# Kernel tuning notes

Hardware: AMD Instinct MI355X
Metric: run time of the kernel (lower is better)

Reference implementation:

```python
import jax, jax.numpy as jnp
import numpy as np

F = 64      # input_v_size
E = 64      # emb_v_size
H = 8       # int(sqrt(emb_v_size))
P = 512     # proj_e_size
B, T = 64, 256


def setup_inputs() -> dict:
    key = jax.random.key(0)
    ks = jax.random.split(key, 14)
    s1 = 1.0            # Linear(1->H): fan_in=1
    s2 = 1.0 / np.sqrt(H)
    s3 = 1.0 / np.sqrt(F * E)
    return {
        "x":    jax.random.normal(ks[0], (B, T, F), dtype=jnp.float32),
        "time": jax.random.uniform(ks[1], (B, T, F), dtype=jnp.float32),
        # stacked per-feature Linear(1->H): weight [F,H], bias [F,H]
        "w1v": jax.random.uniform(ks[2], (F, H), jnp.float32, -s1, s1),
        "b1v": jax.random.uniform(ks[3], (F, H), jnp.float32, -s1, s1),
        # stacked per-feature Linear(H->E, bias=False): [F,H,E]
        "w2v": jax.random.uniform(ks[4], (F, H, E), jnp.float32, -s2, s2),
        "w1t": jax.random.uniform(ks[5], (F, H), jnp.float32, -s1, s1),
        "b1t": jax.random.uniform(ks[6], (F, H), jnp.float32, -s1, s1),
        "w2t": jax.random.uniform(ks[7], (F, H, E), jnp.float32, -s2, s2),
        # Wx, Wt: Linear(F*E -> P) stored as [F*E, P] (= torch weight.T)
        "wx":  jax.random.uniform(ks[8], (F * E, P), jnp.float32, -s3, s3),
        "bx":  jax.random.uniform(ks[9], (P,), jnp.float32, -s3, s3),
        "wt":  jax.random.uniform(ks[10], (F * E, P), jnp.float32, -s3, s3),
        "bt":  jax.random.uniform(ks[11], (P,), jnp.float32, -s3, s3),
    }


def _branch(inp, w1, b1, w2):
    # inp [B,T,F]; w1,b1 [F,H]; w2 [F,H,E]
    h = jnp.tanh(inp[..., None] * w1 + b1)          # [B,T,F,H]
    e = jnp.einsum("btfh,fhe->btfe", h, w2)          # [B,T,F,E]
    return e.reshape(*inp.shape[:2], -1)              # [B,T,F*E]


def reference(x, time, w1v, b1v, w2v, w1t, b1t, w2t, wx, bx, wt, bt):
    x_out = _branch(x, w1v, b1v, w2v)
    t_out = _branch(time, w1t, b1t, w2t)
    return (x_out @ wx + bx) + (t_out @ wt + bt)      # [B,T,P]
```

## Files before the change

kernel.cpp:

```cpp
#include <hip/hip_runtime.h>
#include <cstdint>
#include <cstddef>

#define FF 64
#define EE 64
#define HH 8
#define PP 512
#define MM 16384
#define KK 1024

typedef __bf16 bf16x8 __attribute__((ext_vector_type(8)));
typedef float  floatx4 __attribute__((ext_vector_type(4)));

__device__ __forceinline__ unsigned short f2bf(float f) {
    unsigned int u = __float_as_uint(f);
    u += 0x7FFFu + ((u >> 16) & 1u);
    return (unsigned short)(u >> 16);
}

__device__ __forceinline__ unsigned pack2(unsigned short a, unsigned short b) {
    return (unsigned)a | ((unsigned)b << 16);
}

__device__ __forceinline__ float fast_tanh_s(float t) {
    float e, r;
    asm("v_exp_f32 %0, %1" : "=v"(e) : "v"(t));
    float d = e + 1.0f;
    asm("v_rcp_f32 %0, %1" : "=v"(r) : "v"(d));
    return __builtin_fmaf(-2.0f, r, 1.0f);
}

__device__ __forceinline__ void gl_lds16(const unsigned short* g, unsigned short* s) {
    __builtin_amdgcn_global_load_lds(
        (__attribute__((address_space(1))) void*)(void*)g,
        (__attribute__((address_space(3))) void*)s,
        16, 0, 0);
}

__global__ __launch_bounds__(256) void combine_kernel(
    const float* __restrict__ w2v, const float* __restrict__ w2t,
    const float* __restrict__ wx,  const float* __restrict__ wt,
    unsigned short* __restrict__ BmatT)
{
    const int tid = threadIdx.x;
    const int bid = blockIdx.x;
    const int br = bid >> 7;
    const int f  = (bid >> 1) & 63;
    const int nh = bid & 1;
    const float* __restrict__ w2 = br ? w2t : w2v;
    const float* __restrict__ W  = br ? wt  : wx;
    __shared__ float w2s[HH * EE];
    for (int i = tid; i < HH * EE; i += 256) w2s[i] = w2[f * HH * EE + i];
    __syncthreads();
    const int n = nh * 256 + tid;
    float acc[HH] = {0,0,0,0,0,0,0,0};
    const float* Wcol = W + (size_t)f * EE * PP + n;
    #pragma unroll 8
    for (int e = 0; e < EE; ++e) {
        const float wv = Wcol[(size_t)e * PP];
        #pragma unroll
        for (int h = 0; h < HH; ++h)
            acc[h] = __builtin_fmaf(w2s[h * EE + e], wv, acc[h]);
    }
    uint4 v;
    v.x = pack2(f2bf(acc[0]), f2bf(acc[1]));
    v.y = pack2(f2bf(acc[2]), f2bf(acc[3]));
    v.z = pack2(f2bf(acc[4]), f2bf(acc[5]));
    v.w = pack2(f2bf(acc[6]), f2bf(acc[7]));
    *reinterpret_cast<uint4*>(&BmatT[(size_t)n * KK + br * 512 + f * 8]) = v;
}

__global__ __launch_bounds__(512, 4) void gemm_fused_kernel(
    const float* __restrict__ x,   const float* __restrict__ tmv,
    const float* __restrict__ w1v, const float* __restrict__ b1v,
    const float* __restrict__ w1t, const float* __restrict__ b1t,
    const unsigned short* __restrict__ Bt,
    const float* __restrict__ bx, const float* __restrict__ bt,
    float* __restrict__ out)
{
    __shared__ __align__(16) unsigned short As[64 * 64];
    __shared__ __align__(16) unsigned short Bs[256 * 64];
    __shared__ __align__(16) float w1s[2 * FF * HH];
    __shared__ __align__(16) float b1s[2 * FF * HH];

    const int tid  = threadIdx.x;
    const int wave = tid >> 6;
    const int lane = tid & 63;
    const int m0 = blockIdx.x * 64;
    const int n0 = blockIdx.y * 256;

    {
        const float c = 2.8853900817779268f;
        #pragma unroll
        for (int t = 0; t < 2; ++t) {
            const int idx = tid + t * 512;
            const int br  = idx >> 9;
            const int rem = idx & 511;
            w1s[idx] = (br ? w1t : w1v)[rem] * c;
            b1s[idx] = (br ? b1t : b1v)[rem] * c;
        }
    }
    __syncthreads();

    const int wm  = wave >> 2;
    const int wn  = wave & 3;
    const int q   = lane >> 4;
    const int ml  = lane & 15;
    const int mlx = ml & 7;
    const int lr  = lane >> 3;
    const int lkg = ((lane & 7) ^ lr) * 8;
    const int fi  = tid & 7;
    const int arow = tid >> 3;
    const int pchunk = (fi ^ (arow & 7)) * 8;

    floatx4 acc[2][4];
    #pragma unroll
    for (int i = 0; i < 2; ++i)
        #pragma unroll
        for (int j = 0; j < 4; ++j)
            acc[i][j] = (floatx4){0.f, 0.f, 0.f, 0.f};

    for (int k0 = 0; k0 < KK; k0 += 64) {
        const int br = k0 >> 9;
        const int f0 = (k0 >> 3) & 63;

        #pragma unroll
        for (int i = 0; i < 4; ++i) {
            const int seg = wave * 4 + i;
            gl_lds16(&Bt[(size_t)(n0 + seg * 8 + lr) * KK + k0 + lkg], &Bs[seg * 512]);
        }

        {
            const float* __restrict__ inp = br ? tmv : x;
            const int f = f0 + fi;
            const float val = inp[(size_t)(m0 + arow) * FF + f];
            const float4 wlo = reinterpret_cast<const float4*>(w1s)[br * 128 + f * 2];
            const float4 whi = reinterpret_cast<const float4*>(w1s)[br * 128 + f * 2 + 1];
            const float4 blo = reinterpret_cast<const float4*>(b1s)[br * 128 + f * 2];
            const float4 bhi = reinterpret_cast<const float4*>(b1s)[br * 128 + f * 2 + 1];
            float hv[8];
            hv[0] = fast_tanh_s(__builtin_fmaf(val, wlo.x, blo.x));
            hv[1] = fast_tanh_s(__builtin_fmaf(val, wlo.y, blo.y));
            hv[2] = fast_tanh_s(__builtin_fmaf(val, wlo.z, blo.z));
            hv[3] = fast_tanh_s(__builtin_fmaf(val, wlo.w, blo.w));
            hv[4] = fast_tanh_s(__builtin_fmaf(val, whi.x, bhi.x));
            hv[5] = fast_tanh_s(__builtin_fmaf(val, whi.y, bhi.y));
            hv[6] = fast_tanh_s(__builtin_fmaf(val, whi.z, bhi.z));
            hv[7] = fast_tanh_s(__builtin_fmaf(val, whi.w, bhi.w));
            uint4 v;
            v.x = pack2(f2bf(hv[0]), f2bf(hv[1]));
            v.y = pack2(f2bf(hv[2]), f2bf(hv[3]));
            v.z = pack2(f2bf(hv[4]), f2bf(hv[5]));
            v.w = pack2(f2bf(hv[6]), f2bf(hv[7]));
            *reinterpret_cast<uint4*>(&As[arow * 64 + pchunk]) = v;
        }
        __syncthreads();

        #pragma unroll
        for (int kk = 0; kk < 64; kk += 32) {
            const int cl = (kk >> 3) + q;
            const int co = (cl ^ mlx) * 8;
            bf16x8 af[2], bfr[4];
            #pragma unroll
            for (int mt = 0; mt < 2; ++mt)
                af[mt] = *reinterpret_cast<const bf16x8*>(
                    &As[(wm * 32 + mt * 16 + ml) * 64 + co]);
            #pragma unroll
            for (int nt = 0; nt < 4; ++nt)
                bfr[nt] = *reinterpret_cast<const bf16x8*>(
                    &Bs[(wn * 64 + nt * 16 + ml) * 64 + co]);
            #pragma unroll
            for (int mt = 0; mt < 2; ++mt)
                #pragma unroll
                for (int nt = 0; nt < 4; ++nt)
                    acc[mt][nt] = __builtin_amdgcn_mfma_f32_16x16x32_bf16(
                        af[mt], bfr[nt], acc[mt][nt], 0, 0, 0);
        }
        __syncthreads();
    }

    float bias[4];
    #pragma unroll
    for (int nt = 0; nt < 4; ++nt) {
        const int n = n0 + wn * 64 + nt * 16 + ml;
        bias[nt] = bx[n] + bt[n];
    }
    #pragma unroll
    for (int mt = 0; mt < 2; ++mt) {
        const int mb = m0 + wm * 32 + mt * 16 + q * 4;
        #pragma unroll
        for (int r = 0; r < 4; ++r) {
            float* orow = out + (size_t)(mb + r) * PP + n0 + wn * 64 + ml;
            #pragma unroll
            for (int nt = 0; nt < 4; ++nt)
                orow[nt * 16] = acc[mt][nt][r] + bias[nt];
        }
    }
}

extern "C" void kernel_launch(void* const* d_in, const int* in_sizes, int n_in,
                              void* d_out, int out_size, void* d_ws, size_t ws_size,
                              hipStream_t stream)
{
    const float* x   = (const float*)d_in[0];
    const float* tmv = (const float*)d_in[1];
    const float* w1v = (const float*)d_in[2];
    const float* b1v = (const float*)d_in[3];
    const float* w2v = (const float*)d_in[4];
    const float* w1t = (const float*)d_in[5];
    const float* b1t = (const float*)d_in[6];
    const float* w2t = (const float*)d_in[7];
    const float* wx  = (const float*)d_in[8];
    const float* bx  = (const float*)d_in[9];
    const float* wt  = (const float*)d_in[10];
    const float* bt  = (const float*)d_in[11];
    float* out = (float*)d_out;

    unsigned short* Bws = (unsigned short*)d_ws;

    combine_kernel<<<256, 256, 0, stream>>>(w2v, w2t, wx, wt, Bws);
    gemm_fused_kernel<<<dim3(MM / 64, PP / 256), 512, 0, stream>>>(
        x, tmv, w1v, b1v, w1t, b1t, Bws, bx, bt, out);
}
```

Measured before the change: 125.6 us.

## Halve GEMM block threads, enlarge per-wave tile, software-pipeline tanh A-tile generation

The fused GEMM now uses 256 threads (4 waves), each wave owning all 64 rows and a 64-column strip, so each wave does a 4x4 MFMA tile instead of 2x4. The tanh/bf16 A-operand for the next k-step is computed in registers between the two MFMA halves of the current step, which overlaps transcendental work with matrix math. Input loads are prefetched one iteration ahead. The cost is higher register pressure (launch bounds 256,3) and fewer waves per block to hide latency.

After: 126.5 us. Within noise of the previous version (+0.7%).

```diff
diff --git a/kernel.cpp b/kernel.cpp
--- a/kernel.cpp
+++ b/kernel.cpp
@@ -70,7 +70,7 @@
     *reinterpret_cast<uint4*>(&BmatT[(size_t)n * KK + br * 512 + f * 8]) = v;
 }
 
-__global__ __launch_bounds__(512, 4) void gemm_fused_kernel(
+__global__ __launch_bounds__(256, 3) void gemm_fused_kernel(
     const float* __restrict__ x,   const float* __restrict__ tmv,
     const float* __restrict__ w1v, const float* __restrict__ b1v,
     const float* __restrict__ w1t, const float* __restrict__ b1t,
@@ -91,86 +91,126 @@
 
     {
         const float c = 2.8853900817779268f;
-        #pragma unroll
-        for (int t = 0; t < 2; ++t) {
-            const int idx = tid + t * 512;
-            const int br  = idx >> 9;
-            const int rem = idx & 511;
-            w1s[idx] = (br ? w1t : w1v)[rem] * c;
-            b1s[idx] = (br ? b1t : b1v)[rem] * c;
-        }
-    }
-    __syncthreads();
-
-    const int wm  = wave >> 2;
-    const int wn  = wave & 3;
+        const float4 wsrc = (tid < 128) ? reinterpret_cast<const float4*>(w1v)[tid]
+                                        : reinterpret_cast<const float4*>(w1t)[tid - 128];
+        const float4 bsrc = (tid < 128) ? reinterpret_cast<const float4*>(b1v)[tid]
+                                        : reinterpret_cast<const float4*>(b1t)[tid - 128];
+        float4 ws, bs;
+        ws.x = wsrc.x * c; ws.y = wsrc.y * c; ws.z = wsrc.z * c; ws.w = wsrc.w * c;
+        bs.x = bsrc.x * c; bs.y = bsrc.y * c; bs.z = bsrc.z * c; bs.w = bsrc.w * c;
+        reinterpret_cast<float4*>(w1s)[tid] = ws;
+        reinterpret_cast<float4*>(b1s)[tid] = bs;
+    }
+
+    const int wn  = wave;
     const int q   = lane >> 4;
     const int ml  = lane & 15;
     const int mlx = ml & 7;
     const int lr  = lane >> 3;
     const int lkg = ((lane & 7) ^ lr) * 8;
     const int fi  = tid & 7;
-    const int arow = tid >> 3;
-    const int pchunk = (fi ^ (arow & 7)) * 8;
-
-    floatx4 acc[2][4];
+    const int g   = tid >> 3;
+    const int pchunkA = (fi ^ (g & 7)) * 8;
+
+    __syncthreads();
+
+    float4 wlo, whi, blo, bhi;
+    float  va, vb;
+    uint4  pa, pb;
+
+    {
+        wlo = reinterpret_cast<const float4*>(w1s)[fi * 2];
+        whi = reinterpret_cast<const float4*>(w1s)[fi * 2 + 1];
+        blo = reinterpret_cast<const float4*>(b1s)[fi * 2];
+        bhi = reinterpret_cast<const float4*>(b1s)[fi * 2 + 1];
+        va = x[(size_t)(m0 + g) * FF + fi];
+        vb = x[(size_t)(m0 + g + 32) * FF + fi];
+    }
+
+    auto tanh_pack = [&](float val) -> uint4 {
+        float hv[8];
+        hv[0] = fast_tanh_s(__builtin_fmaf(val, wlo.x, blo.x));
+        hv[1] = fast_tanh_s(__builtin_fmaf(val, wlo.y, blo.y));
+        hv[2] = fast_tanh_s(__builtin_fmaf(val, wlo.z, blo.z));
+        hv[3] = fast_tanh_s(__builtin_fmaf(val, wlo.w, blo.w));
+        hv[4] = fast_tanh_s(__builtin_fmaf(val, whi.x, bhi.x));
+        hv[5] = fast_tanh_s(__builtin_fmaf(val, whi.y, bhi.y));
+        hv[6] = fast_tanh_s(__builtin_fmaf(val, whi.z, bhi.z));
+        hv[7] = fast_tanh_s(__builtin_fmaf(val, whi.w, bhi.w));
+        uint4 v;
+        v.x = pack2(f2bf(hv[0]), f2bf(hv[1]));
+        v.y = pack2(f2bf(hv[2]), f2bf(hv[3]));
+        v.z = pack2(f2bf(hv[4]), f2bf(hv[5]));
+        v.w = pack2(f2bf(hv[6]), f2bf(hv[7]));
+        return v;
+    };
+    pa = tanh_pack(va);
+    pb = tanh_pack(vb);
+
+    floatx4 acc[4][4];
     #pragma unroll
-    for (int i = 0; i < 2; ++i)
+    for (int i = 0; i < 4; ++i)
         #pragma unroll
         for (int j = 0; j < 4; ++j)
             acc[i][j] = (floatx4){0.f, 0.f, 0.f, 0.f};
 
-    for (int k0 = 0; k0 < KK; k0 += 64) {
-        const int br = k0 >> 9;
-        const int f0 = (k0 >> 3) & 63;
-
-        #pragma unroll
-        for (int i = 0; i < 4; ++i) {
-            const int seg = wave * 4 + i;
+    for (int it = 0; it < 16; ++it) {
+        const int k0 = it * 64;
+
+        #pragma unroll
+        for (int i = 0; i < 8; ++i) {
+            const int seg = wave * 8 + i;
             gl_lds16(&Bt[(size_t)(n0 + seg * 8 + lr) * KK + k0 + lkg], &Bs[seg * 512]);
         }
+        *reinterpret_cast<uint4*>(&As[g * 64 + pchunkA])        = pa;
+        *reinterpret_cast<uint4*>(&As[(g + 32) * 64 + pchunkA]) = pb;
+
+        const int itn = (it < 15) ? it + 1 : 15;
+        const int brn = itn >> 3;
+        const int fn  = ((itn & 7) << 3) + fi;
+        const float* __restrict__ inpn = brn ? tmv : x;
+        const float nva = inpn[(size_t)(m0 + g) * FF + fn];
+        const float nvb = inpn[(size_t)(m0 + g + 32) * FF + fn];
+        const float4 nwlo = reinterpret_cast<const float4*>(w1s)[brn * 128 + fn * 2];
+        const float4 nwhi = reinterpret_cast<const float4*>(w1s)[brn * 128 + fn * 2 + 1];
+        const float4 nblo = reinterpret_cast<const float4*>(b1s)[brn * 128 + fn * 2];
+        const float4 nbhi = reinterpret_cast<const float4*>(b1s)[brn * 128 + fn * 2 + 1];
+
+        __syncthreads();
+
+        wlo = nwlo; whi = nwhi; blo = nblo; bhi = nbhi;
+        va = nva; vb = nvb;
 
         {
-            const float* __restrict__ inp = br ? tmv : x;
-            const int f = f0 + fi;
-            const float val = inp[(size_t)(m0 + arow) * FF + f];
-            const float4 wlo = reinterpret_cast<const float4*>(w1s)[br * 128 + f * 2];
-            const float4 whi = reinterpret_cast<const float4*>(w1s)[br * 128 + f * 2 + 1];
-            const float4 blo = reinterpret_cast<const float4*>(b1s)[br * 128 + f * 2];
-            const float4 bhi = reinterpret_cast<const float4*>(b1s)[br * 128 + f * 2 + 1];
-            float hv[8];
-            hv[0] = fast_tanh_s(__builtin_fmaf(val, wlo.x, blo.x));
-            hv[1] = fast_tanh_s(__builtin_fmaf(val, wlo.y, blo.y));
-            hv[2] = fast_tanh_s(__builtin_fmaf(val, wlo.z, blo.z));
-            hv[3] = fast_tanh_s(__builtin_fmaf(val, wlo.w, blo.w));
-            hv[4] = fast_tanh_s(__builtin_fmaf(val, whi.x, bhi.x));
-            hv[5] = fast_tanh_s(__builtin_fmaf(val, whi.y, bhi.y));
-            hv[6] = fast_tanh_s(__builtin_fmaf(val, whi.z, bhi.z));
-            hv[7] = fast_tanh_s(__builtin_fmaf(val, whi.w, bhi.w));
-            uint4 v;
-            v.x = pack2(f2bf(hv[0]), f2bf(hv[1]));
-            v.y = pack2(f2bf(hv[2]), f2bf(hv[3]));
-            v.z = pack2(f2bf(hv[4]), f2bf(hv[5]));
-            v.w = pack2(f2bf(hv[6]), f2bf(hv[7]));
-            *reinterpret_cast<uint4*>(&As[arow * 64 + pchunk]) = v;
-        }
-        __syncthreads();
-
-        #pragma unroll
-        for (int kk = 0; kk < 64; kk += 32) {
-            const int cl = (kk >> 3) + q;
-            const int co = (cl ^ mlx) * 8;
-            bf16x8 af[2], bfr[4];
-            #pragma unroll
-            for (int mt = 0; mt < 2; ++mt)
-                af[mt] = *reinterpret_cast<const bf16x8*>(
-                    &As[(wm * 32 + mt * 16 + ml) * 64 + co]);
+            const int co0 = ((0 + q) ^ mlx) * 8;
+            bf16x8 af[4], bfr[4];
+            #pragma unroll
+            for (int mt = 0; mt < 4; ++mt)
+                af[mt] = *reinterpret_cast<const bf16x8*>(&As[(mt * 16 + ml) * 64 + co0]);
             #pragma unroll
             for (int nt = 0; nt < 4; ++nt)
                 bfr[nt] = *reinterpret_cast<const bf16x8*>(
-                    &Bs[(wn * 64 + nt * 16 + ml) * 64 + co]);
-            #pragma unroll
-            for (int mt = 0; mt < 2; ++mt)
+                    &Bs[(wn * 64 + nt * 16 + ml) * 64 + co0]);
+            #pragma unroll
+            for (int mt = 0; mt < 4; ++mt)
+                #pragma unroll
+                for (int nt = 0; nt < 4; ++nt)
+                    acc[mt][nt] = __builtin_amdgcn_mfma_f32_16x16x32_bf16(
+                        af[mt], bfr[nt], acc[mt][nt], 0, 0, 0);
+
+            pa = tanh_pack(va);
+            pb = tanh_pack(vb);
+
+            const int co1 = ((4 + q) ^ mlx) * 8;
+            #pragma unroll
+            for (int mt = 0; mt < 4; ++mt)
+                af[mt] = *reinterpret_cast<const bf16x8*>(&As[(mt * 16 + ml) * 64 + co1]);
+            #pragma unroll
+            for (int nt = 0; nt < 4; ++nt)
+                bfr[nt] = *reinterpret_cast<const bf16x8*>(
+                    &Bs[(wn * 64 + nt * 16 + ml) * 64 + co1]);
+            #pragma unroll
+            for (int mt = 0; mt < 4; ++mt)
                 #pragma unroll
                 for (int nt = 0; nt < 4; ++nt)
                     acc[mt][nt] = __builtin_amdgcn_mfma_f32_16x16x32_bf16(
@@ -186,8 +226,8 @@
         bias[nt] = bx[n] + bt[n];
     }
     #pragma unroll
-    for (int mt = 0; mt < 2; ++mt) {
-        const int mb = m0 + wm * 32 + mt * 16 + q * 4;
+    for (int mt = 0; mt < 4; ++mt) {
+        const int mb = m0 + mt * 16 + q * 4;
         #pragma unroll
         for (int r = 0; r < 4; ++r) {
             float* orow = out + (size_t)(mb + r) * PP + n0 + wn * 64 + ml;
@@ -219,6 +259,6 @@
     unsigned short* Bws = (unsigned short*)d_ws;
 
     combine_kernel<<<256, 256, 0, stream>>>(w2v, w2t, wx, wt, Bws);
-    gemm_fused_kernel<<<dim3(MM / 64, PP / 256), 512, 0, stream>>>(
+    gemm_fused_kernel<<<dim3(MM / 64, PP / 256), 256, 0, stream>>>(
         x, tmv, w1v, b1v, w1t, b1t, Bws, bx, bt, out);
 }
```
